# Kernel optimization log

Hardware: AMD Instinct MI355X
Metric: run time of the kernel (lower is better)

Reference implementation:

```python
import jax, jax.numpy as jnp
import numpy as np

DEG = 2
KNOTS = (0.25, 0.5, 0.75)
CONDITION_DIM = 1
INPUT_DIM = 1024
OUTPUT_DIM = 1024
NUM_BASIS = DEG + 1 + len(KNOTS)  # 6
BATCH = 32768


def setup_inputs() -> dict:
    key = jax.random.key(0)
    k1, k2, k3 = jax.random.split(key, 3)
    # x carries [features | condition] concatenated along dim 1
    x = jax.random.uniform(k1, (BATCH, INPUT_DIM + CONDITION_DIM), dtype=jnp.float32)
    fan_in = INPUT_DIM  # kaiming-style scale for the weight tensor
    weight = jax.random.normal(k2, (NUM_BASIS * CONDITION_DIM, INPUT_DIM, OUTPUT_DIM), dtype=jnp.float32) / np.sqrt(fan_in)
    bias_param = jax.random.normal(k3, (OUTPUT_DIM,), dtype=jnp.float32) / np.sqrt(fan_in)
    return {"x": x, "weight": weight, "bias_param": bias_param}


def _basis(condition):
    # condition: (B, condition_dim). Truncated power spline basis per condition column.
    cols = []
    for j in range(CONDITION_DIM):
        t = condition[:, j]
        for i in range(DEG + 1):
            cols.append(t ** i)
        for knot in KNOTS:
            cols.append(jax.nn.relu(t - knot) ** DEG)
    return jnp.stack(cols, axis=1)  # (B, coef_dim)


def reference(x, weight, bias_param):
    feats = x[:, :INPUT_DIM]            # (B, d)
    condition = x[:, INPUT_DIM:]        # (B, condition_dim)
    basis = _basis(condition)           # (B, c)
    # Same math as einsum('bc,cde->bde') then ('bde,bd->be'), but contracted in
    # the cheaper order (avoids the (B, d, e) per-sample weight tensor):
    xw = jnp.einsum('bd,cde->bce', feats, weight)   # (B, c, e)
    out = jnp.einsum('bc,bce->be', basis, xw)       # (B, e)
    return out + bias_param
```

## Files before the change

### kernel.cpp

```cpp
#include <hip/hip_runtime.h>
#include <stdint.h>

#define IN_DIM    1024
#define OUT_DIM   1024
#define ROWSTRIDE 1025
#define BATCH     32768
#define NBASIS    6
#define KTOT      (NBASIS * IN_DIM)
#define KSTEPS    96

typedef __bf16 bf16x8 __attribute__((ext_vector_type(8)));
typedef float  f32x4  __attribute__((ext_vector_type(4)));

__device__ inline unsigned short f2bf(float f) {
  union { float f; unsigned u; } v; v.f = f;
  unsigned u = v.u;
  return (unsigned short)((u + 0x7FFFu + ((u >> 16) & 1u)) >> 16);
}

__global__ void prep_f(const float* __restrict__ x,
                       unsigned short* __restrict__ F,
                       float* __restrict__ bas_t) {
  const int b = blockIdx.x;
  const int tid = threadIdx.x;
  const float* xr = x + (size_t)b * ROWSTRIDE;
  unsigned short* frow = F + (size_t)b * IN_DIM;

  #pragma unroll
  for (int k = 0; k < 2; ++k) {
    int d = k * 512 + tid * 2;
    union { unsigned short u[2]; unsigned int w; } p;
    p.u[0] = f2bf(xr[d]);
    p.u[1] = f2bf(xr[d + 1]);
    *(unsigned int*)(frow + d) = p.w;
  }

  if (tid < 6) {
    float t  = xr[IN_DIM];
    float r1 = fmaxf(t - 0.25f, 0.0f);
    float r2 = fmaxf(t - 0.50f, 0.0f);
    float r3 = fmaxf(t - 0.75f, 0.0f);
    float v = (tid == 0) ? 1.0f
            : (tid == 1) ? t
            : (tid == 2) ? t * t
            : (tid == 3) ? r1 * r1
            : (tid == 4) ? r2 * r2
            :              r3 * r3;
    bas_t[(size_t)tid * BATCH + b] = v;
  }
}

__global__ void prep_wt(const float* __restrict__ w, unsigned short* __restrict__ bt) {
  __shared__ unsigned short t[32][33];
  int k0 = blockIdx.x * 32;
  int e0 = blockIdx.y * 32;
  int tid = threadIdx.x;
  #pragma unroll
  for (int p = tid; p < 1024; p += 256) {
    int kk = p >> 5, ee = p & 31;
    t[ee][kk] = f2bf(w[(size_t)(k0 + kk) * OUT_DIM + e0 + ee]);
  }
  __syncthreads();
  #pragma unroll
  for (int p = tid; p < 1024; p += 256) {
    int ee = p >> 5, kk = p & 31;
    bt[(size_t)(e0 + ee) * KTOT + k0 + kk] = t[ee][kk];
  }
}

__device__ inline void gload_lds16(const unsigned short* g, unsigned short* l) {
  __builtin_amdgcn_global_load_lds((const __attribute__((address_space(1))) void*)g,
                                   (__attribute__((address_space(3))) void*)l, 16, 0, 0);
}

__global__ __launch_bounds__(256, 2) void vcl_gemm(
    const unsigned short* __restrict__ F,
    const unsigned short* __restrict__ BT,
    const float* __restrict__ bas_t,
    const float* __restrict__ bias,
    float* __restrict__ out) {
  __shared__ unsigned short smem[2 * 128 * 64];
  __shared__ __align__(16) float bas_lds[NBASIS * 128];
  unsigned short* sA = smem;
  unsigned short* sB = smem + 128 * 64;

  const int tid = threadIdx.x;
  const int bm0 = (blockIdx.x >> 3) * 128;
  const int bn0 = (blockIdx.x & 7) * 128;

  const int wv   = tid >> 6;
  const int lane = tid & 63;
  const int lr   = lane >> 3;
  const int kc   = (lane & 7) ^ lr;
  const int ln15 = lane & 15;
  const int quad = lane >> 4;
  const int wm   = wv >> 1, wn = wv & 1;
  const int cs0  = quad ^ (ln15 & 7);
  const int cs1  = (4 + quad) ^ (ln15 & 7);

  for (int p = tid; p < NBASIS * 128; p += 256)
    bas_lds[p] = bas_t[(size_t)(p >> 7) * BATCH + bm0 + (p & 127)];

  const unsigned short* gA[4];
  const unsigned short* gB[4];
  unsigned short* lA[4];
  unsigned short* lB[4];
  #pragma unroll
  for (int wc = 0; wc < 4; ++wc) {
    int r = wv * 32 + wc * 8 + lr;
    gA[wc] = F  + (size_t)(bm0 + r) * IN_DIM + kc * 8;
    gB[wc] = BT + (size_t)(bn0 + r) * KTOT   + kc * 8;
    lA[wc] = sA + (wv * 4 + wc) * 512;
    lB[wc] = sB + (wv * 4 + wc) * 512;
  }

  float bias_j[4];
  #pragma unroll
  for (int j = 0; j < 4; ++j)
    bias_j[j] = bias[bn0 + wn * 64 + j * 16 + ln15];

  f32x4 acc[4][4]  = {};
  f32x4 accO[4][4] = {};

  #pragma unroll
  for (int wc = 0; wc < 4; ++wc) {
    gload_lds16(gA[wc], lA[wc]);
    gload_lds16(gB[wc], lB[wc]);
  }

  for (int t = 0; t < KSTEPS; ++t) {
    __syncthreads();

    bf16x8 bfr2[2][4];
    #pragma unroll
    for (int j = 0; j < 4; ++j) {
      int nt = wn * 64 + j * 16 + ln15;
      bfr2[0][j] = *(const bf16x8*)(sB + nt * 64 + cs0 * 8);
      bfr2[1][j] = *(const bf16x8*)(sB + nt * 64 + cs1 * 8);
    }
    #pragma unroll
    for (int i = 0; i < 4; ++i) {
      int rowt = wm * 64 + i * 16 + ln15;
      bf16x8 af0 = *(const bf16x8*)(sA + rowt * 64 + cs0 * 8);
      bf16x8 af1 = *(const bf16x8*)(sA + rowt * 64 + cs1 * 8);
      #pragma unroll
      for (int j = 0; j < 4; ++j) {
        acc[i][j] = __builtin_amdgcn_mfma_f32_16x16x32_bf16(af0, bfr2[0][j], acc[i][j], 0, 0, 0);
        acc[i][j] = __builtin_amdgcn_mfma_f32_16x16x32_bf16(af1, bfr2[1][j], acc[i][j], 0, 0, 0);
      }
    }

    __syncthreads();
    if (t + 1 < KSTEPS) {
      const int offA = ((t + 1) & 15) * 64;
      const int offB = (t + 1) * 64;
      #pragma unroll
      for (int wc = 0; wc < 4; ++wc) {
        gload_lds16(gA[wc] + offA, lA[wc]);
        gload_lds16(gB[wc] + offB, lB[wc]);
      }
    }

    if ((t & 15) == 15) {
      const int c = t >> 4;
      #pragma unroll
      for (int i = 0; i < 4; ++i) {
        f32x4 bb = *(const f32x4*)(&bas_lds[c * 128 + wm * 64 + i * 16 + quad * 4]);
        #pragma unroll
        for (int j = 0; j < 4; ++j) {
          #pragma unroll
          for (int r = 0; r < 4; ++r)
            accO[i][j][r] += bb[r] * acc[i][j][r];
          acc[i][j] = (f32x4){0.0f, 0.0f, 0.0f, 0.0f};
        }
      }
    }
  }

  float* buf = (float*)smem;
  const int ROWP = 132;
  const int erow = tid >> 3;
  const int echk = tid & 7;
  const int grow_base = bm0 + (erow >> 4) * 64 + (erow & 15);
  const int gcol = bn0 + echk * 16;

  #pragma unroll
  for (int i = 0; i < 4; ++i) {
    __syncthreads();
    #pragma unroll
    for (int j = 0; j < 4; ++j) {
      int cr = wm * 16 + quad * 4;
      int cc = wn * 64 + j * 16 + ln15;
      #pragma unroll
      for (int r = 0; r < 4; ++r)
        buf[(cr + r) * ROWP + cc] = accO[i][j][r] + bias_j[j];
    }
    __syncthreads();
    float* orow = out + (size_t)(grow_base + i * 16) * OUT_DIM + gcol;
    const float* brow = buf + erow * ROWP + echk * 16;
    #pragma unroll
    for (int e = 0; e < 4; ++e)
      *(f32x4*)(orow + e * 4) = *(const f32x4*)(brow + e * 4);
  }
}

extern "C" void kernel_launch(void* const* d_in, const int* in_sizes, int n_in,
                              void* d_out, int out_size, void* d_ws, size_t ws_size,
                              hipStream_t stream) {
  const float* x    = (const float*)d_in[0];
  const float* w    = (const float*)d_in[1];
  const float* bias = (const float*)d_in[2];
  float* out = (float*)d_out;

  unsigned short* F  = (unsigned short*)d_ws;
  unsigned short* BT = (unsigned short*)((char*)d_ws + (size_t)BATCH * IN_DIM * 2);
  float* bas_t = (float*)((char*)d_ws + (size_t)BATCH * IN_DIM * 2 + (size_t)OUT_DIM * KTOT * 2);

  prep_f<<<BATCH, 256, 0, stream>>>(x, F, bas_t);
  dim3 g2(KTOT / 32, OUT_DIM / 32);
  prep_wt<<<g2, 256, 0, stream>>>(w, BT);
  vcl_gemm<<<(BATCH / 128) * (OUT_DIM / 128), 256, 0, stream>>>(F, BT, bas_t, bias, out);
}
```

Measured before the change: 692.9 us.

## Fold basis scaling into A tile and enlarge GEMM tile to 256x256

The GEMM moves from 128x128 tiles with 256 threads to 256x256 tiles with 512 threads and double-buffered LDS. The A operand is now loaded through registers and scaled by the per-row basis value before being written to LDS, so a single accumulator set replaces the per-basis partial accumulators and their periodic merges. MFMA clusters are interleaved with split prefetches under s_setprio and explicit barriers. prep_f becomes a grid-stride kernel with fewer blocks. The larger tile raises data reuse, but it uses 128KB of LDS, which may limit occupancy, and it adds a bf16 rounding step on the scaled A values.

```diff
diff --git a/kernel.cpp b/kernel.cpp
--- a/kernel.cpp
+++ b/kernel.cpp
@@ -18,35 +18,34 @@
   return (unsigned short)((u + 0x7FFFu + ((u >> 16) & 1u)) >> 16);
 }
 
-__global__ void prep_f(const float* __restrict__ x,
-                       unsigned short* __restrict__ F,
-                       float* __restrict__ bas_t) {
-  const int b = blockIdx.x;
+__global__ __launch_bounds__(256) void prep_f(const float* __restrict__ x,
+                                              unsigned short* __restrict__ F,
+                                              float* __restrict__ bas_t) {
   const int tid = threadIdx.x;
-  const float* xr = x + (size_t)b * ROWSTRIDE;
-  unsigned short* frow = F + (size_t)b * IN_DIM;
-
-  #pragma unroll
-  for (int k = 0; k < 2; ++k) {
-    int d = k * 512 + tid * 2;
-    union { unsigned short u[2]; unsigned int w; } p;
-    p.u[0] = f2bf(xr[d]);
-    p.u[1] = f2bf(xr[d + 1]);
-    *(unsigned int*)(frow + d) = p.w;
-  }
-
-  if (tid < 6) {
-    float t  = xr[IN_DIM];
-    float r1 = fmaxf(t - 0.25f, 0.0f);
-    float r2 = fmaxf(t - 0.50f, 0.0f);
-    float r3 = fmaxf(t - 0.75f, 0.0f);
-    float v = (tid == 0) ? 1.0f
-            : (tid == 1) ? t
-            : (tid == 2) ? t * t
-            : (tid == 3) ? r1 * r1
-            : (tid == 4) ? r2 * r2
-            :              r3 * r3;
-    bas_t[(size_t)tid * BATCH + b] = v;
+  const int rl  = tid >> 7;
+  const int j   = tid & 127;
+  for (int rb = blockIdx.x * 2 + rl; rb < BATCH; rb += 4096) {
+    const float* xr = x + (size_t)rb * ROWSTRIDE;
+    unsigned short* fr = F + (size_t)rb * IN_DIM;
+    #pragma unroll
+    for (int i = 0; i < 4; ++i) {
+      float v0 = xr[2 * j + 256 * i];
+      float v1 = xr[2 * j + 1 + 256 * i];
+      unsigned pw = (unsigned)f2bf(v0) | ((unsigned)f2bf(v1) << 16);
+      *(unsigned*)(fr + 2 * j + 256 * i) = pw;
+    }
+    if (j == 0) {
+      float t  = xr[IN_DIM];
+      float r1 = fmaxf(t - 0.25f, 0.0f);
+      float r2 = fmaxf(t - 0.50f, 0.0f);
+      float r3 = fmaxf(t - 0.75f, 0.0f);
+      bas_t[rb]             = 1.0f;
+      bas_t[BATCH + rb]     = t;
+      bas_t[2 * BATCH + rb] = t * t;
+      bas_t[3 * BATCH + rb] = r1 * r1;
+      bas_t[4 * BATCH + rb] = r2 * r2;
+      bas_t[5 * BATCH + rb] = r3 * r3;
+    }
   }
 }
 
@@ -73,133 +72,183 @@
                                    (__attribute__((address_space(3))) void*)l, 16, 0, 0);
 }
 
-__global__ __launch_bounds__(256, 2) void vcl_gemm(
+__device__ __attribute__((always_inline)) inline
+void scale_store(uint4 w, float s, unsigned short* dst) {
+  bf16x8 r;
+  unsigned q0 = w.x, q1 = w.y, q2 = w.z, q3 = w.w;
+  r[0] = (__bf16)(__uint_as_float(q0 << 16) * s);
+  r[1] = (__bf16)(__uint_as_float(q0 & 0xFFFF0000u) * s);
+  r[2] = (__bf16)(__uint_as_float(q1 << 16) * s);
+  r[3] = (__bf16)(__uint_as_float(q1 & 0xFFFF0000u) * s);
+  r[4] = (__bf16)(__uint_as_float(q2 << 16) * s);
+  r[5] = (__bf16)(__uint_as_float(q2 & 0xFFFF0000u) * s);
+  r[6] = (__bf16)(__uint_as_float(q3 << 16) * s);
+  r[7] = (__bf16)(__uint_as_float(q3 & 0xFFFF0000u) * s);
+  *(bf16x8*)dst = r;
+}
+
+template<int I0>
+__device__ __attribute__((always_inline)) inline
+void cluster(f32x4 (&acc)[8][4], const bf16x8* afr, const bf16x8* bfr) {
+  __builtin_amdgcn_s_setprio(1);
+  #pragma unroll
+  for (int i = 0; i < 4; ++i) {
+    #pragma unroll
+    for (int j = 0; j < 4; ++j)
+      acc[I0 + i][j] =
+          __builtin_amdgcn_mfma_f32_16x16x32_bf16(afr[i], bfr[j], acc[I0 + i][j], 0, 0, 0);
+  }
+  __builtin_amdgcn_s_setprio(0);
+}
+
+__global__ __launch_bounds__(512, 2) void vcl_gemm(
     const unsigned short* __restrict__ F,
     const unsigned short* __restrict__ BT,
     const float* __restrict__ bas_t,
     const float* __restrict__ bias,
     float* __restrict__ out) {
-  __shared__ unsigned short smem[2 * 128 * 64];
-  __shared__ __align__(16) float bas_lds[NBASIS * 128];
-  unsigned short* sA = smem;
-  unsigned short* sB = smem + 128 * 64;
-
-  const int tid = threadIdx.x;
-  const int bm0 = (blockIdx.x >> 3) * 128;
-  const int bn0 = (blockIdx.x & 7) * 128;
-
+  __shared__ __align__(16) unsigned short smem[65536];
+  unsigned short* const sA0 = smem;
+  unsigned short* const sA1 = smem + 16384;
+  unsigned short* const sB0 = smem + 32768;
+  unsigned short* const sB1 = smem + 49152;
+
+  const int tid  = threadIdx.x;
   const int wv   = tid >> 6;
   const int lane = tid & 63;
-  const int lr   = lane >> 3;
-  const int kc   = (lane & 7) ^ lr;
   const int ln15 = lane & 15;
   const int quad = lane >> 4;
-  const int wm   = wv >> 1, wn = wv & 1;
-  const int cs0  = quad ^ (ln15 & 7);
-  const int cs1  = (4 + quad) ^ (ln15 & 7);
-
-  for (int p = tid; p < NBASIS * 128; p += 256)
-    bas_lds[p] = bas_t[(size_t)(p >> 7) * BATCH + bm0 + (p & 127)];
-
-  const unsigned short* gA[4];
-  const unsigned short* gB[4];
-  unsigned short* lA[4];
-  unsigned short* lB[4];
-  #pragma unroll
-  for (int wc = 0; wc < 4; ++wc) {
-    int r = wv * 32 + wc * 8 + lr;
-    gA[wc] = F  + (size_t)(bm0 + r) * IN_DIM + kc * 8;
-    gB[wc] = BT + (size_t)(bn0 + r) * KTOT   + kc * 8;
-    lA[wc] = sA + (wv * 4 + wc) * 512;
-    lB[wc] = sB + (wv * 4 + wc) * 512;
-  }
+  const int lr   = lane >> 3;
+  const int kg   = lane & 7;
+  const int wm   = wv >> 2;
+  const int wn   = wv & 3;
+
+  const int bm0 = (blockIdx.x >> 2) * 256;
+  const int bn0 = (blockIdx.x & 3) * 256;
+
+  int arow[4]; unsigned agoff[4]; int awoff[4];
+  const unsigned short* gB[4]; int lboff[4];
+  #pragma unroll
+  for (int w = 0; w < 4; ++w) {
+    arow[w]  = wv * 32 + w * 8 + lr;
+    agoff[w] = (unsigned)(bm0 + arow[w]) * 1024u + (unsigned)(kg * 8);
+    awoff[w] = arow[w] * 128 + ((kg ^ lr) << 4);
+    gB[w]    = BT + (size_t)(bn0 + arow[w]) * KTOT + (kg ^ lr) * 8;
+    lboff[w] = (wv * 4 + w) * 512;
+  }
+
+  const int slot0 = quad ^ (ln15 & 7);
+  const int aoff0 = (wm * 128 + ln15) * 64 + slot0 * 8;
+  const int boff0 = (wn * 64 + ln15) * 64 + slot0 * 8;
 
   float bias_j[4];
   #pragma unroll
-  for (int j = 0; j < 4; ++j)
-    bias_j[j] = bias[bn0 + wn * 64 + j * 16 + ln15];
-
-  f32x4 acc[4][4]  = {};
-  f32x4 accO[4][4] = {};
-
-  #pragma unroll
-  for (int wc = 0; wc < 4; ++wc) {
-    gload_lds16(gA[wc], lA[wc]);
-    gload_lds16(gB[wc], lB[wc]);
+  for (int jj = 0; jj < 4; ++jj) bias_j[jj] = bias[bn0 + wn * 64 + jj * 16 + ln15];
+
+  float s_[4];
+  #pragma unroll
+  for (int w = 0; w < 4; ++w) s_[w] = bas_t[bm0 + arow[w]];
+
+  f32x4 acc[8][4] = {};
+
+  {
+    uint4 ad[4];
+    #pragma unroll
+    for (int w = 0; w < 4; ++w) ad[w] = *(const uint4*)(F + agoff[w]);
+    #pragma unroll
+    for (int w = 0; w < 4; ++w) gload_lds16(gB[w], sB0 + lboff[w]);
+    #pragma unroll
+    for (int w = 0; w < 4; ++w)
+      scale_store(ad[w], s_[w], (unsigned short*)((char*)sA0 + awoff[w]));
+    asm volatile("s_waitcnt vmcnt(0) lgkmcnt(0)" ::: "memory");
+    __builtin_amdgcn_s_barrier();
   }
 
   for (int t = 0; t < KSTEPS; ++t) {
+    const unsigned short* sAc = (t & 1) ? sA1 : sA0;
+    const unsigned short* sBc = (t & 1) ? sB1 : sB0;
+    unsigned short* sAn = (t & 1) ? sA0 : sA1;
+    unsigned short* sBn = (t & 1) ? sB0 : sB1;
+    const int tn = (t + 1 == KSTEPS) ? 0 : (t + 1);
+    const int doffA = (tn & 15) * 64;
+    const unsigned offB = (unsigned)(tn * 64);
+
+    if ((tn & 15) == 0) {
+      const int c = tn >> 4;
+      #pragma unroll
+      for (int w = 0; w < 4; ++w)
+        s_[w] = bas_t[(size_t)c * BATCH + bm0 + arow[w]];
+    }
+
+    uint4 ad[4];
+    bf16x8 afr[4], bfr[4];
+
+    #pragma unroll
+    for (int j = 0; j < 4; ++j) bfr[j] = *(const bf16x8*)(sBc + boff0 + j * 1024);
+    #pragma unroll
+    for (int i = 0; i < 4; ++i) afr[i] = *(const bf16x8*)(sAc + aoff0 + i * 1024);
+    #pragma unroll
+    for (int w = 0; w < 4; ++w) ad[w] = *(const uint4*)(F + agoff[w] + doffA);
+    gload_lds16(gB[0] + offB, sBn + lboff[0]);
+    gload_lds16(gB[1] + offB, sBn + lboff[1]);
+    __builtin_amdgcn_s_barrier();
+    cluster<0>(acc, afr, bfr);
+    __builtin_amdgcn_s_barrier();
+
+    #pragma unroll
+    for (int i = 0; i < 4; ++i) afr[i] = *(const bf16x8*)(sAc + aoff0 + (i + 4) * 1024);
+    gload_lds16(gB[2] + offB, sBn + lboff[2]);
+    gload_lds16(gB[3] + offB, sBn + lboff[3]);
+    __builtin_amdgcn_s_barrier();
+    cluster<4>(acc, afr, bfr);
+    __builtin_amdgcn_s_barrier();
+
+    #pragma unroll
+    for (int j = 0; j < 4; ++j) bfr[j] = *(const bf16x8*)(sBc + (boff0 ^ 32) + j * 1024);
+    #pragma unroll
+    for (int i = 0; i < 4; ++i) afr[i] = *(const bf16x8*)(sAc + (aoff0 ^ 32) + i * 1024);
+    __builtin_amdgcn_s_barrier();
+    cluster<0>(acc, afr, bfr);
+    scale_store(ad[0], s_[0], (unsigned short*)((char*)sAn + awoff[0]));
+    scale_store(ad[1], s_[1], (unsigned short*)((char*)sAn + awoff[1]));
+    __builtin_amdgcn_s_barrier();
+
+    #pragma unroll
+    for (int i = 0; i < 4; ++i) afr[i] = *(const bf16x8*)(sAc + (aoff0 ^ 32) + (i + 4) * 1024);
+    __builtin_amdgcn_s_barrier();
+    cluster<4>(acc, afr, bfr);
+    scale_store(ad[2], s_[2], (unsigned short*)((char*)sAn + awoff[2]));
+    scale_store(ad[3], s_[3], (unsigned short*)((char*)sAn + awoff[3]));
+    asm volatile("s_waitcnt vmcnt(0) lgkmcnt(0)" ::: "memory");
+    __builtin_amdgcn_s_barrier();
+  }
+
+  float* buf = (float*)smem;
+  const int ROWP = 260;
+  const int erow = tid >> 3;
+  const int echk = tid & 7;
+
+  #pragma unroll
+  for (int g = 0; g < 4; ++g) {
     __syncthreads();
-
-    bf16x8 bfr2[2][4];
-    #pragma unroll
-    for (int j = 0; j < 4; ++j) {
-      int nt = wn * 64 + j * 16 + ln15;
-      bfr2[0][j] = *(const bf16x8*)(sB + nt * 64 + cs0 * 8);
-      bfr2[1][j] = *(const bf16x8*)(sB + nt * 64 + cs1 * 8);
-    }
-    #pragma unroll
-    for (int i = 0; i < 4; ++i) {
-      int rowt = wm * 64 + i * 16 + ln15;
-      bf16x8 af0 = *(const bf16x8*)(sA + rowt * 64 + cs0 * 8);
-      bf16x8 af1 = *(const bf16x8*)(sA + rowt * 64 + cs1 * 8);
+    if (wm == (g >> 1)) {
+      const int i0 = (g & 1) * 4;
       #pragma unroll
-      for (int j = 0; j < 4; ++j) {
-        acc[i][j] = __builtin_amdgcn_mfma_f32_16x16x32_bf16(af0, bfr2[0][j], acc[i][j], 0, 0, 0);
-        acc[i][j] = __builtin_amdgcn_mfma_f32_16x16x32_bf16(af1, bfr2[1][j], acc[i][j], 0, 0, 0);
-      }
-    }
-
-    __syncthreads();
-    if (t + 1 < KSTEPS) {
-      const int offA = ((t + 1) & 15) * 64;
-      const int offB = (t + 1) * 64;
-      #pragma unroll
-      for (int wc = 0; wc < 4; ++wc) {
-        gload_lds16(gA[wc] + offA, lA[wc]);
-        gload_lds16(gB[wc] + offB, lB[wc]);
-      }
-    }
-
-    if ((t & 15) == 15) {
-      const int c = t >> 4;
-      #pragma unroll
-      for (int i = 0; i < 4; ++i) {
-        f32x4 bb = *(const f32x4*)(&bas_lds[c * 128 + wm * 64 + i * 16 + quad * 4]);
+      for (int ii = 0; ii < 4; ++ii) {
         #pragma unroll
         for (int j = 0; j < 4; ++j) {
           #pragma unroll
           for (int r = 0; r < 4; ++r)
-            accO[i][j][r] += bb[r] * acc[i][j][r];
-          acc[i][j] = (f32x4){0.0f, 0.0f, 0.0f, 0.0f};
+            buf[(ii * 16 + quad * 4 + r) * ROWP + wn * 64 + j * 16 + ln15] =
+                acc[i0 + ii][j][r] + bias_j[j];
         }
       }
     }
-  }
-
-  float* buf = (float*)smem;
-  const int ROWP = 132;
-  const int erow = tid >> 3;
-  const int echk = tid & 7;
-  const int grow_base = bm0 + (erow >> 4) * 64 + (erow & 15);
-  const int gcol = bn0 + echk * 16;
-
-  #pragma unroll
-  for (int i = 0; i < 4; ++i) {
     __syncthreads();
-    #pragma unroll
-    for (int j = 0; j < 4; ++j) {
-      int cr = wm * 16 + quad * 4;
-      int cc = wn * 64 + j * 16 + ln15;
-      #pragma unroll
-      for (int r = 0; r < 4; ++r)
-        buf[(cr + r) * ROWP + cc] = accO[i][j][r] + bias_j[j];
-    }
-    __syncthreads();
-    float* orow = out + (size_t)(grow_base + i * 16) * OUT_DIM + gcol;
-    const float* brow = buf + erow * ROWP + echk * 16;
-    #pragma unroll
-    for (int e = 0; e < 4; ++e)
+    float* orow = out + (size_t)(bm0 + g * 64 + erow) * OUT_DIM + bn0 + echk * 32;
+    const float* brow = buf + erow * ROWP + echk * 32;
+    #pragma unroll
+    for (int e = 0; e < 8; ++e)
       *(f32x4*)(orow + e * 4) = *(const f32x4*)(brow + e * 4);
   }
 }
@@ -216,8 +265,8 @@
   unsigned short* BT = (unsigned short*)((char*)d_ws + (size_t)BATCH * IN_DIM * 2);
   float* bas_t = (float*)((char*)d_ws + (size_t)BATCH * IN_DIM * 2 + (size_t)OUT_DIM * KTOT * 2);
 
-  prep_f<<<BATCH, 256, 0, stream>>>(x, F, bas_t);
+  prep_f<<<2048, 256, 0, stream>>>(x, F, bas_t);
   dim3 g2(KTOT / 32, OUT_DIM / 32);
   prep_wt<<<g2, 256, 0, stream>>>(w, BT);
-  vcl_gemm<<<(BATCH / 128) * (OUT_DIM / 128), 256, 0, stream>>>(F, BT, bas_t, bias, out);
-}
+  vcl_gemm<<<(BATCH / 256) * (OUT_DIM / 256), 512, 0, stream>>>(F, BT, bas_t, bias, out);
+}
```

Measured after the change: 695.0 us. Within noise of the previous version (+0.3%).
